# Optimization experiments

Hardware: AMD Instinct MI355X
Metric: run time of the kernel (lower is better)

The kernel has to match this reference:

```python
import jax, jax.numpy as jnp
import numpy as np


def setup_inputs() -> dict:
    key = jax.random.key(0)
    k1, k2 = jax.random.split(key)
    d, T, n = 256, 8192, 64
    # scale down so exp(ht^T D^T D hj) stays in range, as typical trained D would
    H = jax.random.normal(k1, (d, T), dtype=jnp.float32) * 0.1
    D = jax.random.normal(k2, (n, d), dtype=jnp.float32) * 0.1
    l2 = jnp.ones((), dtype=jnp.float32)
    return {"H": H, "D": D, "l2": l2}


def reference(H, D, l2):
    # H: [d, T], D: [n, d]
    DH = D @ H                                   # [n, T] = D @ H_T.T
    # S[t, j] = h_t^T (D^T D) h_j  == (DH)^T (DH)
    S = jnp.einsum('nt,nj->tj', DH, DH)          # [T, T]
    # beta_j = exp(-0.5 * ||D h_j||^2); row t: attn[t,:] = beta * exp(S[t,:]) / sum
    log_beta = -0.5 * jnp.sum(DH * DH, axis=0)   # [T]
    attn_map = jax.nn.softmax(S + log_beta[None, :], axis=1)  # [T, T]
    Z = l2 * (H @ attn_map)                      # [d, T]
    return Z
```

## Files before the change

### kernel.cpp

```cpp
#include <hip/hip_runtime.h>

#define T_DIM 8192
#define D_DIM 256
#define N_DIM 64
#define LOG2E 1.44269504f

typedef __bf16 bf16x8 __attribute__((ext_vector_type(8)));
typedef __bf16 bf16x4 __attribute__((ext_vector_type(4)));
typedef float f32x16 __attribute__((ext_vector_type(16)));

__device__ __forceinline__ f32x16 zero16() {
  f32x16 v;
#pragma unroll
  for (int i = 0; i < 16; ++i) v[i] = 0.f;
  return v;
}


__global__ __launch_bounds__(256) void k_dh(const float* __restrict__ H,
                                            const float* __restrict__ Dm,
                                            __bf16* __restrict__ DHf,
                                            float* __restrict__ lbe,
                                            float* __restrict__ rowsum) {
  __shared__ __bf16 HlThi[64 * 264];
  __shared__ __bf16 HlTlo[64 * 264];
  __shared__ __bf16 DHs[64 * 72];
  const int tid = threadIdx.x;
  const int t0 = blockIdx.x * 64;
  const int lane = tid & 63;
  const int wave = tid >> 6;
  const int h = lane >> 5;
  const int l31 = lane & 31;
  const float4* H4 = (const float4*)H;
#pragma unroll
  for (int r = 0; r < 16; ++r) {
    int idx = r * 256 + tid;
    int d = idx >> 4, tc = idx & 15;
    float4 v = H4[(size_t)d * (T_DIM / 4) + (t0 >> 2) + tc];
    float vv[4] = {v.x, v.y, v.z, v.w};
#pragma unroll
    for (int i = 0; i < 4; ++i) {
      __bf16 hi = (__bf16)vv[i];
      float lo = vv[i] - (float)hi;
      HlThi[(tc * 4 + i) * 264 + d] = hi;
      HlTlo[(tc * 4 + i) * 264 + d] = (__bf16)lo;
    }
  }
  __syncthreads();
  const int tt = wave & 1, nh = wave >> 1;
  const int m = tt * 32 + l31;
  const int n = nh * 32 + l31;
  f32x16 c = zero16();
  for (int kk = 0; kk < 16; ++kk) {
    bf16x8 ahi = *(const bf16x8*)&HlThi[m * 264 + kk * 16 + h * 8];
    bf16x8 alo = *(const bf16x8*)&HlTlo[m * 264 + kk * 16 + h * 8];
    const float4* dp = (const float4*)(Dm + (size_t)n * 256 + kk * 16 + h * 8);
    float4 b0 = dp[0], b1 = dp[1];
    float bv[8] = {b0.x, b0.y, b0.z, b0.w, b1.x, b1.y, b1.z, b1.w};
    bf16x8 bhi, blo;
#pragma unroll
    for (int i = 0; i < 8; ++i) {
      __bf16 hi = (__bf16)bv[i];
      bhi[i] = hi;
      blo[i] = (__bf16)(bv[i] - (float)hi);
    }
    c = __builtin_amdgcn_mfma_f32_32x32x16_bf16(ahi, bhi, c, 0, 0, 0);
    c = __builtin_amdgcn_mfma_f32_32x32x16_bf16(ahi, blo, c, 0, 0, 0);
    c = __builtin_amdgcn_mfma_f32_32x32x16_bf16(alo, bhi, c, 0, 0, 0);
  }
#pragma unroll
  for (int r = 0; r < 16; ++r) {
    int row = tt * 32 + (r & 3) + 8 * (r >> 2) + 4 * h;
    DHs[row * 72 + n] = (__bf16)c[r];
  }
  __syncthreads();
#pragma unroll
  for (int r = 0; r < 2; ++r) {
    int idx = r * 256 + tid;
    int g = idx >> 8, cc = (idx >> 5) & 7, l = idx & 31;
    bf16x8 w = *(const bf16x8*)&DHs[(g * 32 + l) * 72 + cc * 8];
    *(bf16x8*)(DHf + (size_t)(blockIdx.x * 2 + g) * 2048 + cc * 256 + l * 8) = w;
  }
  if (tid < 64) {
    float s = 0.f;
#pragma unroll
    for (int q = 0; q < 8; ++q) {
      bf16x8 w = *(const bf16x8*)&DHs[tid * 72 + q * 8];
#pragma unroll
      for (int i = 0; i < 8; ++i) { float f = (float)w[i]; s += f * f; }
    }
    lbe[t0 + tid] = -0.5f * s * LOG2E;
    rowsum[t0 + tid] = 0.f;
  }
}

__global__ __launch_bounds__(512, 4) void k_rowsum(const __bf16* __restrict__ DHf,
                                                   const float* __restrict__ lbe,
                                                   float* __restrict__ rowsum) {
  __shared__ float red2[256][33];
  const int tid = threadIdx.x;
  const int lane = tid & 63;
  const int wave = tid >> 6;
  const int h = lane >> 5;
  const int l31 = lane & 31;
  const int t0 = (int)(blockIdx.x >> 4) * 256;
  const int jbase = (int)(blockIdx.x & 15) * 512;
  const size_t Gt = (size_t)(t0 >> 5) + wave;
  bf16x8 aR[4];
#pragma unroll
  for (int kk = 0; kk < 4; ++kk)
    aR[kk] = *(const bf16x8*)(DHf + Gt * 2048 + kk * 512 + lane * 8);
  float racc[16];
#pragma unroll
  for (int r = 0; r < 16; ++r) racc[r] = 0.f;
  bf16x8 b[4];
  {
    const size_t Gj = (size_t)(jbase >> 5);
#pragma unroll
    for (int kk = 0; kk < 4; ++kk)
      b[kk] = *(const bf16x8*)(DHf + Gj * 2048 + kk * 512 + lane * 8);
  }
  for (int jit = 0; jit < 16; ++jit) {
    bf16x8 bn[4];
    if (jit < 15) {
      const size_t Gj = (size_t)(jbase >> 5) + jit + 1;
#pragma unroll
      for (int kk = 0; kk < 4; ++kk)
        bn[kk] = *(const bf16x8*)(DHf + Gj * 2048 + kk * 512 + lane * 8);
    }
    const float lbv = lbe[jbase + jit * 32 + l31];
    f32x16 s = zero16();
    s = __builtin_amdgcn_mfma_f32_32x32x16_bf16(aR[0], b[0], s, 0, 0, 0);
    s = __builtin_amdgcn_mfma_f32_32x32x16_bf16(aR[1], b[1], s, 0, 0, 0);
    s = __builtin_amdgcn_mfma_f32_32x32x16_bf16(aR[2], b[2], s, 0, 0, 0);
    s = __builtin_amdgcn_mfma_f32_32x32x16_bf16(aR[3], b[3], s, 0, 0, 0);
#pragma unroll
    for (int r = 0; r < 16; ++r)
      racc[r] += __builtin_amdgcn_exp2f(__builtin_fmaf(s[r], LOG2E, lbv));
    if (jit < 15) {
#pragma unroll
      for (int kk = 0; kk < 4; ++kk) b[kk] = bn[kk];
    }
  }
#pragma unroll
  for (int r = 0; r < 16; ++r) {
    int tl = wave * 32 + (r & 3) + 8 * (r >> 2) + 4 * h;
    red2[tl][l31] = racc[r];
  }
  __syncthreads();
  if (tid < 256) {
    float s = 0.f;
#pragma unroll 8
    for (int c = 0; c < 32; ++c) s += red2[tid][c];
    atomicAdd(&rowsum[t0 + tid], s);
  }
}

__global__ __launch_bounds__(256) void k_scaleH(const float* __restrict__ H,
                                                const float* __restrict__ rowsum,
                                                __bf16* __restrict__ Hbf_sw) {
  __shared__ float rinvL[64];
  const int tid = threadIdx.x;
  const int bx = blockIdx.x;
  const int tblk = bx >> 1, dh = bx & 1;
  const int t0 = tblk * 64;
  if (tid < 64) rinvL[tid] = 1.0f / rowsum[t0 + tid];
  __syncthreads();
#pragma unroll
  for (int itr = 0; itr < 4; ++itr) {
    int idx = itr * 256 + tid;
    int dl = idx >> 3, tbp = idx & 7;
    int d = dh * 128 + dl;
    int swz = (d ^ (d >> 3)) & 7;
    int tloc = (tbp ^ swz) << 3;
    const float4* hp = (const float4*)(H + (size_t)d * T_DIM + t0 + tloc);
    float4 v0 = hp[0], v1 = hp[1];
    float4 r0 = *(const float4*)&rinvL[tloc];
    float4 r1 = *(const float4*)&rinvL[tloc + 4];
    bf16x8 w;
    w[0] = (__bf16)(v0.x * r0.x); w[1] = (__bf16)(v0.y * r0.y);
    w[2] = (__bf16)(v0.z * r0.z); w[3] = (__bf16)(v0.w * r0.w);
    w[4] = (__bf16)(v1.x * r1.x); w[5] = (__bf16)(v1.y * r1.y);
    w[6] = (__bf16)(v1.z * r1.z); w[7] = (__bf16)(v1.w * r1.w);
    *(bf16x8*)(Hbf_sw + (size_t)tblk * 16384 + (size_t)d * 64 + tbp * 8) = w;
  }
}

__global__ __launch_bounds__(256, 2) void k_z(const __bf16* __restrict__ Hbf_sw,
                                              const __bf16* __restrict__ DHf,
                                              const float* __restrict__ lbe,
                                              float* __restrict__ Zp) {
  __shared__ __bf16 Hs[2][128 * 64];
  __shared__ __bf16 Pt[2][128 * 64];
  const int tid = threadIdx.x;
  const int lane = tid & 63;
  const int wave = tid >> 6;
  const int h = lane >> 5;
  const int l31 = lane & 31;
  const int bx = blockIdx.x;
  const int ts = bx & 3;
  const int dh = (bx >> 2) & 1;
  const int j0 = (bx >> 3) * 128;
  const int s_tt = wave & 1, s_jg = wave >> 1;
  bf16x8 bS[2][4];
  float lbv[2];
#pragma unroll
  for (int q = 0; q < 2; ++q) {
    const size_t Gj = (j0 >> 5) + s_jg * 2 + q;
#pragma unroll
    for (int kk = 0; kk < 4; ++kk)
      bS[q][kk] = *(const bf16x8*)(DHf + Gj * 2048 + kk * 512 + lane * 8);
    lbv[q] = lbe[j0 + (s_jg * 2 + q) * 32 + l31];
  }
  f32x16 acc[2][2];
#pragma unroll
  for (int u = 0; u < 2; ++u)
#pragma unroll
    for (int v = 0; v < 2; ++v) acc[u][v] = zero16();

#define DMA_HS(buf_, it_)                                                       \
  {                                                                             \
    const __bf16* gsrc =                                                        \
        Hbf_sw + (size_t)(ts * 32 + (it_)) * 16384 + (size_t)dh * 8192;         \
    _Pragma("unroll") for (int r = 0; r < 4; ++r) {                             \
      int chunk = wave * 4 + r;                                                 \
      __builtin_amdgcn_global_load_lds(                                         \
          (const __attribute__((address_space(1))) unsigned int*)(gsrc +        \
              chunk * 512 + lane * 8),                                          \
          (__attribute__((address_space(3))) unsigned int*)(&Hs[buf_][0] +      \
              chunk * 512),                                                     \
          16, 0, 0);                                                            \
    }                                                                           \
  }

#define LOAD_AR(reg_, n_)                                                       \
  {                                                                             \
    const size_t Gt_ = (size_t)(ts * 64 + (n_)*2 + s_tt);                       \
    _Pragma("unroll") for (int kk = 0; kk < 4; ++kk)                            \
        (reg_)[kk] = *(const bf16x8*)(DHf + Gt_ * 2048 + kk * 512 + lane * 8);  \
  }

#define S_PHASE(p_, reg_)                                                       \
  {                                                                             \
    _Pragma("unroll") for (int q = 0; q < 2; ++q) {                             \
      f32x16 s = zero16();                                                      \
      _Pragma("unroll") for (int kk = 0; kk < 4; ++kk)                          \
          s = __builtin_amdgcn_mfma_f32_32x32x16_bf16((reg_)[kk], bS[q][kk], s, \
                                                      0, 0, 0);                 \
      const int jl = (s_jg * 2 + q) * 32 + l31;                                 \
      const int sj = (jl ^ (jl >> 3)) & 7;                                      \
      _Pragma("unroll") for (int g = 0; g < 4; ++g) {                           \
        const int tl = s_tt * 32 + g * 8 + 4 * h;                               \
        bf16x4 pv;                                                              \
        pv[0] = (__bf16)__builtin_amdgcn_exp2f(                                 \
            __builtin_fmaf(s[g * 4 + 0], LOG2E, lbv[q]));                       \
        pv[1] = (__bf16)__builtin_amdgcn_exp2f(                                 \
            __builtin_fmaf(s[g * 4 + 1], LOG2E, lbv[q]));                       \
        pv[2] = (__bf16)__builtin_amdgcn_exp2f(                                 \
            __builtin_fmaf(s[g * 4 + 2], LOG2E, lbv[q]));                       \
        pv[3] = (__bf16)__builtin_amdgcn_exp2f(                                 \
            __builtin_fmaf(s[g * 4 + 3], LOG2E, lbv[q]));                       \
        const int cchunk = tl >> 3;                                             \
        *(bf16x4*)&Pt[p_][jl * 64 + ((cchunk ^ sj) << 3) + 4 * h] = pv;         \
      }                                                                         \
    }                                                                           \
  }

#define Z_PHASE(p_)                                                             \
  {                                                                             \
    __builtin_amdgcn_s_setprio(1);                                              \
    _Pragma("unroll") for (int kk = 0; kk < 4; ++kk) {                          \
      const int c = kk * 2 + h;                                                 \
      bf16x8 af[2], bw[2];                                                      \
      _Pragma("unroll") for (int u = 0; u < 2; ++u) {                           \
        int dl = (wave & 1) * 64 + u * 32 + l31;                                \
        af[u] =                                                                 \
            *(const bf16x8*)&Hs[p_][dl * 64 + ((c ^ ((dl ^ (dl >> 3)) & 7)) << 3)]; \
      }                                                                         \
      _Pragma("unroll") for (int v = 0; v < 2; ++v) {                           \
        int j = (wave >> 1) * 64 + v * 32 + l31;                                \
        bw[v] =                                                                 \
            *(const bf16x8*)&Pt[p_][j * 64 + ((c ^ ((j ^ (j >> 3)) & 7)) << 3)]; \
      }                                                                         \
      _Pragma("unroll") for (int u = 0; u < 2; ++u)                             \
          _Pragma("unroll") for (int v = 0; v < 2; ++v)                         \
              acc[u][v] = __builtin_amdgcn_mfma_f32_32x32x16_bf16(              \
                  af[u], bw[v], acc[u][v], 0, 0, 0);                            \
    }                                                                           \
    __builtin_amdgcn_s_setprio(0);                                              \
  }

  bf16x8 aR[4], aRn[4];
  LOAD_AR(aR, 0);
  DMA_HS(0, 0);
  S_PHASE(0, aR);
  LOAD_AR(aRn, 1);
  __syncthreads();

  for (int ii = 0; ii < 16; ++ii) {
    const int it0 = ii * 2;
    DMA_HS(1, it0 + 1);
    if (it0 < 30) LOAD_AR(aR, it0 + 2);
    S_PHASE(1, aRn);
    Z_PHASE(0);
    __syncthreads();
    if (it0 + 1 < 31) {
      DMA_HS(0, it0 + 2);
      S_PHASE(0, aR);
    }
    if (it0 + 1 < 30) LOAD_AR(aRn, it0 + 3);
    Z_PHASE(1);
    __syncthreads();
  }
#undef Z_PHASE
#undef S_PHASE
#undef LOAD_AR
#undef DMA_HS
  float* zp = Zp + (size_t)ts * (256 * (size_t)T_DIM);
#pragma unroll
  for (int u = 0; u < 2; ++u)
#pragma unroll
    for (int v = 0; v < 2; ++v)
#pragma unroll
      for (int r = 0; r < 16; ++r) {
        int d = dh * 128 + (wave & 1) * 64 + u * 32 + (r & 3) + 8 * (r >> 2) + 4 * h;
        int j = j0 + (wave >> 1) * 64 + v * 32 + l31;
        zp[(size_t)d * T_DIM + j] = acc[u][v][r];
      }
}

__global__ __launch_bounds__(256) void k_zred(const float* __restrict__ Zp,
                                              const float* __restrict__ l2p,
                                              float* __restrict__ Z) {
  const int i = blockIdx.x * 256 + threadIdx.x;
  const float l2v = l2p[0];
  const float4* zp4 = (const float4*)Zp;
  float4 a = zp4[i];
#pragma unroll
  for (int s = 1; s < 4; ++s) {
    float4 b = zp4[(size_t)s * 524288 + i];
    a.x += b.x; a.y += b.y; a.z += b.z; a.w += b.w;
  }
  float4 o = {a.x * l2v, a.y * l2v, a.z * l2v, a.w * l2v};
  ((float4*)Z)[i] = o;
}

extern "C" void kernel_launch(void* const* d_in, const int* in_sizes, int n_in,
                              void* d_out, int out_size, void* d_ws,
                              size_t ws_size, hipStream_t stream) {
  (void)in_sizes; (void)n_in; (void)out_size; (void)ws_size;
  const float* H = (const float*)d_in[0];
  const float* Dm = (const float*)d_in[1];
  const float* l2 = (const float*)d_in[2];
  float* Z = (float*)d_out;
  char* ws = (char*)d_ws;
  __bf16* DHf = (__bf16*)ws;
  float* lbe = (float*)(ws + 1048576);
  float* rowsum = (float*)(ws + 1048576 + 32768);
  __bf16* Hbf_sw = (__bf16*)(ws + 1114112);
  float* Zp = (float*)(ws + 5308416);

  k_dh<<<128, 256, 0, stream>>>(H, Dm, DHf, lbe, rowsum);
  k_rowsum<<<512, 512, 0, stream>>>(DHf, lbe, rowsum);
  k_scaleH<<<256, 256, 0, stream>>>(H, rowsum, Hbf_sw);
  k_z<<<512, 256, 0, stream>>>(Hbf_sw, DHf, lbe, Zp);
  k_zred<<<2048, 256, 0, stream>>>(Zp, l2, Z);
}
```

Before: 145.7 us.

## Fuse five kernels into one persistent kernel with grid-wide barriers

Merges the DH, rowsum, scale-H, Z and Z-reduction kernels into a single 512-block launch, separating stages with a hierarchical atomic grid barrier. The barrier counters are reset with a memset. The goal is to remove per-kernel launch gaps and tail effects. In exchange, every stage is forced to the same block count and shared-memory union, the DH stage now reads H directly from global memory with strided scalar loads instead of going through LDS, and correctness depends on all 512 blocks being co-resident.

```diff
diff --git a/kernel.cpp b/kernel.cpp
--- a/kernel.cpp
+++ b/kernel.cpp
@@ -16,207 +16,216 @@
   return v;
 }
 
-
-__global__ __launch_bounds__(256) void k_dh(const float* __restrict__ H,
-                                            const float* __restrict__ Dm,
-                                            __bf16* __restrict__ DHf,
-                                            float* __restrict__ lbe,
-                                            float* __restrict__ rowsum) {
-  __shared__ __bf16 HlThi[64 * 264];
-  __shared__ __bf16 HlTlo[64 * 264];
-  __shared__ __bf16 DHs[64 * 72];
+__device__ __forceinline__ void gbar(unsigned int* bar, int slot) {
+  __syncthreads();
+  if (threadIdx.x == 0) {
+    __threadfence();
+    const int bx = (int)blockIdx.x;
+    unsigned int o = __hip_atomic_fetch_add(&bar[16 + slot * 8 + (bx & 7)], 1u,
+                                            __ATOMIC_ACQ_REL,
+                                            __HIP_MEMORY_SCOPE_AGENT);
+    if (o == 63u) {
+      unsigned int r = __hip_atomic_fetch_add(&bar[slot], 1u, __ATOMIC_ACQ_REL,
+                                              __HIP_MEMORY_SCOPE_AGENT);
+      if (r == 7u)
+        __hip_atomic_store(&bar[8 + slot], 1u, __ATOMIC_RELEASE,
+                           __HIP_MEMORY_SCOPE_AGENT);
+    }
+    while (__hip_atomic_load(&bar[8 + slot], __ATOMIC_RELAXED,
+                             __HIP_MEMORY_SCOPE_AGENT) == 0u)
+      __builtin_amdgcn_s_sleep(8);
+    __threadfence();
+  }
+  __syncthreads();
+}
+
+union SMem {
+  struct {
+    __bf16 Hs[2][8192];
+    __bf16 Pt[2][8192];
+  } z;
+  __bf16 DHs[64 * 72];
+  float red2[128][33];
+  float rinvL[64];
+};
+
+__global__ __launch_bounds__(256, 2) void k_fused(
+    const float* __restrict__ H, const float* __restrict__ Dm,
+    const float* __restrict__ l2p, float* __restrict__ Z,
+    __bf16* __restrict__ DHf, float* __restrict__ lbe,
+    float* __restrict__ rowsum, __bf16* __restrict__ Hbf_sw,
+    float* __restrict__ Zp, unsigned int* __restrict__ bar) {
+  __shared__ SMem smem;
   const int tid = threadIdx.x;
-  const int t0 = blockIdx.x * 64;
+  const int bx = (int)blockIdx.x;
   const int lane = tid & 63;
   const int wave = tid >> 6;
   const int h = lane >> 5;
   const int l31 = lane & 31;
-  const float4* H4 = (const float4*)H;
-#pragma unroll
-  for (int r = 0; r < 16; ++r) {
-    int idx = r * 256 + tid;
-    int d = idx >> 4, tc = idx & 15;
-    float4 v = H4[(size_t)d * (T_DIM / 4) + (t0 >> 2) + tc];
-    float vv[4] = {v.x, v.y, v.z, v.w};
-#pragma unroll
-    for (int i = 0; i < 4; ++i) {
-      __bf16 hi = (__bf16)vv[i];
-      float lo = vv[i] - (float)hi;
-      HlThi[(tc * 4 + i) * 264 + d] = hi;
-      HlTlo[(tc * 4 + i) * 264 + d] = (__bf16)lo;
-    }
-  }
-  __syncthreads();
-  const int tt = wave & 1, nh = wave >> 1;
-  const int m = tt * 32 + l31;
-  const int n = nh * 32 + l31;
-  f32x16 c = zero16();
-  for (int kk = 0; kk < 16; ++kk) {
-    bf16x8 ahi = *(const bf16x8*)&HlThi[m * 264 + kk * 16 + h * 8];
-    bf16x8 alo = *(const bf16x8*)&HlTlo[m * 264 + kk * 16 + h * 8];
-    const float4* dp = (const float4*)(Dm + (size_t)n * 256 + kk * 16 + h * 8);
-    float4 b0 = dp[0], b1 = dp[1];
-    float bv[8] = {b0.x, b0.y, b0.z, b0.w, b1.x, b1.y, b1.z, b1.w};
-    bf16x8 bhi, blo;
-#pragma unroll
-    for (int i = 0; i < 8; ++i) {
-      __bf16 hi = (__bf16)bv[i];
-      bhi[i] = hi;
-      blo[i] = (__bf16)(bv[i] - (float)hi);
-    }
-    c = __builtin_amdgcn_mfma_f32_32x32x16_bf16(ahi, bhi, c, 0, 0, 0);
-    c = __builtin_amdgcn_mfma_f32_32x32x16_bf16(ahi, blo, c, 0, 0, 0);
-    c = __builtin_amdgcn_mfma_f32_32x32x16_bf16(alo, bhi, c, 0, 0, 0);
-  }
-#pragma unroll
-  for (int r = 0; r < 16; ++r) {
-    int row = tt * 32 + (r & 3) + 8 * (r >> 2) + 4 * h;
-    DHs[row * 72 + n] = (__bf16)c[r];
-  }
-  __syncthreads();
-#pragma unroll
-  for (int r = 0; r < 2; ++r) {
-    int idx = r * 256 + tid;
-    int g = idx >> 8, cc = (idx >> 5) & 7, l = idx & 31;
-    bf16x8 w = *(const bf16x8*)&DHs[(g * 32 + l) * 72 + cc * 8];
-    *(bf16x8*)(DHf + (size_t)(blockIdx.x * 2 + g) * 2048 + cc * 256 + l * 8) = w;
-  }
-  if (tid < 64) {
-    float s = 0.f;
-#pragma unroll
-    for (int q = 0; q < 8; ++q) {
-      bf16x8 w = *(const bf16x8*)&DHs[tid * 72 + q * 8];
-#pragma unroll
-      for (int i = 0; i < 8; ++i) { float f = (float)w[i]; s += f * f; }
-    }
-    lbe[t0 + tid] = -0.5f * s * LOG2E;
-    rowsum[t0 + tid] = 0.f;
-  }
-}
-
-__global__ __launch_bounds__(512, 4) void k_rowsum(const __bf16* __restrict__ DHf,
-                                                   const float* __restrict__ lbe,
-                                                   float* __restrict__ rowsum) {
-  __shared__ float red2[256][33];
-  const int tid = threadIdx.x;
-  const int lane = tid & 63;
-  const int wave = tid >> 6;
-  const int h = lane >> 5;
-  const int l31 = lane & 31;
-  const int t0 = (int)(blockIdx.x >> 4) * 256;
-  const int jbase = (int)(blockIdx.x & 15) * 512;
-  const size_t Gt = (size_t)(t0 >> 5) + wave;
-  bf16x8 aR[4];
-#pragma unroll
-  for (int kk = 0; kk < 4; ++kk)
-    aR[kk] = *(const bf16x8*)(DHf + Gt * 2048 + kk * 512 + lane * 8);
-  float racc[16];
-#pragma unroll
-  for (int r = 0; r < 16; ++r) racc[r] = 0.f;
-  bf16x8 b[4];
+
+  if (bx < 128) {
+    const int t0 = bx * 64;
+    const int tt = wave & 1, nh = wave >> 1;
+    const int m = tt * 32 + l31;
+    const int n = nh * 32 + l31;
+    f32x16 c = zero16();
+    for (int kk = 0; kk < 16; ++kk) {
+      float av[8];
+#pragma unroll
+      for (int e = 0; e < 8; ++e)
+        av[e] = H[(size_t)(kk * 16 + h * 8 + e) * T_DIM + t0 + m];
+      bf16x8 ahi, alo;
+#pragma unroll
+      for (int e = 0; e < 8; ++e) {
+        __bf16 hi = (__bf16)av[e];
+        ahi[e] = hi;
+        alo[e] = (__bf16)(av[e] - (float)hi);
+      }
+      const float4* dp = (const float4*)(Dm + (size_t)n * 256 + kk * 16 + h * 8);
+      float4 b0 = dp[0], b1 = dp[1];
+      float bv[8] = {b0.x, b0.y, b0.z, b0.w, b1.x, b1.y, b1.z, b1.w};
+      bf16x8 bhi, blo;
+#pragma unroll
+      for (int i = 0; i < 8; ++i) {
+        __bf16 hi = (__bf16)bv[i];
+        bhi[i] = hi;
+        blo[i] = (__bf16)(bv[i] - (float)hi);
+      }
+      c = __builtin_amdgcn_mfma_f32_32x32x16_bf16(ahi, bhi, c, 0, 0, 0);
+      c = __builtin_amdgcn_mfma_f32_32x32x16_bf16(ahi, blo, c, 0, 0, 0);
+      c = __builtin_amdgcn_mfma_f32_32x32x16_bf16(alo, bhi, c, 0, 0, 0);
+    }
+#pragma unroll
+    for (int r = 0; r < 16; ++r) {
+      int row = tt * 32 + (r & 3) + 8 * (r >> 2) + 4 * h;
+      smem.DHs[row * 72 + n] = (__bf16)c[r];
+    }
+    __syncthreads();
+#pragma unroll
+    for (int r = 0; r < 2; ++r) {
+      int idx = r * 256 + tid;
+      int g = idx >> 8, cc = (idx >> 5) & 7, l = idx & 31;
+      bf16x8 w = *(const bf16x8*)&smem.DHs[(g * 32 + l) * 72 + cc * 8];
+      *(bf16x8*)(DHf + (size_t)(bx * 2 + g) * 2048 + cc * 256 + l * 8) = w;
+    }
+    if (tid < 64) {
+      float s = 0.f;
+#pragma unroll
+      for (int q = 0; q < 8; ++q) {
+        bf16x8 w = *(const bf16x8*)&smem.DHs[tid * 72 + q * 8];
+#pragma unroll
+        for (int i = 0; i < 8; ++i) { float f = (float)w[i]; s += f * f; }
+      }
+      lbe[t0 + tid] = -0.5f * s * LOG2E;
+      rowsum[t0 + tid] = 0.f;
+    }
+  }
+  gbar(bar, 0);
+
   {
-    const size_t Gj = (size_t)(jbase >> 5);
+    const int t0 = (bx >> 3) * 128;
+    const int jbase = (bx & 7) * 1024;
+    const size_t Gt = (size_t)(t0 >> 5) + wave;
+    bf16x8 aR[4];
 #pragma unroll
     for (int kk = 0; kk < 4; ++kk)
-      b[kk] = *(const bf16x8*)(DHf + Gj * 2048 + kk * 512 + lane * 8);
-  }
-  for (int jit = 0; jit < 16; ++jit) {
-    bf16x8 bn[4];
-    if (jit < 15) {
-      const size_t Gj = (size_t)(jbase >> 5) + jit + 1;
+      aR[kk] = *(const bf16x8*)(DHf + Gt * 2048 + kk * 512 + lane * 8);
+    float racc[16];
+#pragma unroll
+    for (int r = 0; r < 16; ++r) racc[r] = 0.f;
+    bf16x8 b[4];
+    {
+      const size_t Gj = (size_t)(jbase >> 5);
 #pragma unroll
       for (int kk = 0; kk < 4; ++kk)
-        bn[kk] = *(const bf16x8*)(DHf + Gj * 2048 + kk * 512 + lane * 8);
-    }
-    const float lbv = lbe[jbase + jit * 32 + l31];
-    f32x16 s = zero16();
-    s = __builtin_amdgcn_mfma_f32_32x32x16_bf16(aR[0], b[0], s, 0, 0, 0);
-    s = __builtin_amdgcn_mfma_f32_32x32x16_bf16(aR[1], b[1], s, 0, 0, 0);
-    s = __builtin_amdgcn_mfma_f32_32x32x16_bf16(aR[2], b[2], s, 0, 0, 0);
-    s = __builtin_amdgcn_mfma_f32_32x32x16_bf16(aR[3], b[3], s, 0, 0, 0);
-#pragma unroll
-    for (int r = 0; r < 16; ++r)
-      racc[r] += __builtin_amdgcn_exp2f(__builtin_fmaf(s[r], LOG2E, lbv));
-    if (jit < 15) {
-#pragma unroll
-      for (int kk = 0; kk < 4; ++kk) b[kk] = bn[kk];
-    }
-  }
-#pragma unroll
-  for (int r = 0; r < 16; ++r) {
-    int tl = wave * 32 + (r & 3) + 8 * (r >> 2) + 4 * h;
-    red2[tl][l31] = racc[r];
-  }
-  __syncthreads();
-  if (tid < 256) {
-    float s = 0.f;
+        b[kk] = *(const bf16x8*)(DHf + Gj * 2048 + kk * 512 + lane * 8);
+    }
+    for (int jit = 0; jit < 32; ++jit) {
+      bf16x8 bn[4];
+      if (jit < 31) {
+        const size_t Gj = (size_t)(jbase >> 5) + jit + 1;
+#pragma unroll
+        for (int kk = 0; kk < 4; ++kk)
+          bn[kk] = *(const bf16x8*)(DHf + Gj * 2048 + kk * 512 + lane * 8);
+      }
+      const float lbv = lbe[jbase + jit * 32 + l31];
+      f32x16 s = zero16();
+      s = __builtin_amdgcn_mfma_f32_32x32x16_bf16(aR[0], b[0], s, 0, 0, 0);
+      s = __builtin_amdgcn_mfma_f32_32x32x16_bf16(aR[1], b[1], s, 0, 0, 0);
+      s = __builtin_amdgcn_mfma_f32_32x32x16_bf16(aR[2], b[2], s, 0, 0, 0);
+      s = __builtin_amdgcn_mfma_f32_32x32x16_bf16(aR[3], b[3], s, 0, 0, 0);
+#pragma unroll
+      for (int r = 0; r < 16; ++r)
+        racc[r] += __builtin_amdgcn_exp2f(__builtin_fmaf(s[r], LOG2E, lbv));
+      if (jit < 31) {
+#pragma unroll
+        for (int kk = 0; kk < 4; ++kk) b[kk] = bn[kk];
+      }
+    }
+#pragma unroll
+    for (int r = 0; r < 16; ++r) {
+      int tl = wave * 32 + (r & 3) + 8 * (r >> 2) + 4 * h;
+      smem.red2[tl][l31] = racc[r];
+    }
+    __syncthreads();
+    if (tid < 128) {
+      float s = 0.f;
 #pragma unroll 8
-    for (int c = 0; c < 32; ++c) s += red2[tid][c];
-    atomicAdd(&rowsum[t0 + tid], s);
-  }
-}
-
-__global__ __launch_bounds__(256) void k_scaleH(const float* __restrict__ H,
-                                                const float* __restrict__ rowsum,
-                                                __bf16* __restrict__ Hbf_sw) {
-  __shared__ float rinvL[64];
-  const int tid = threadIdx.x;
-  const int bx = blockIdx.x;
-  const int tblk = bx >> 1, dh = bx & 1;
-  const int t0 = tblk * 64;
-  if (tid < 64) rinvL[tid] = 1.0f / rowsum[t0 + tid];
-  __syncthreads();
-#pragma unroll
-  for (int itr = 0; itr < 4; ++itr) {
-    int idx = itr * 256 + tid;
-    int dl = idx >> 3, tbp = idx & 7;
-    int d = dh * 128 + dl;
-    int swz = (d ^ (d >> 3)) & 7;
-    int tloc = (tbp ^ swz) << 3;
-    const float4* hp = (const float4*)(H + (size_t)d * T_DIM + t0 + tloc);
-    float4 v0 = hp[0], v1 = hp[1];
-    float4 r0 = *(const float4*)&rinvL[tloc];
-    float4 r1 = *(const float4*)&rinvL[tloc + 4];
-    bf16x8 w;
-    w[0] = (__bf16)(v0.x * r0.x); w[1] = (__bf16)(v0.y * r0.y);
-    w[2] = (__bf16)(v0.z * r0.z); w[3] = (__bf16)(v0.w * r0.w);
-    w[4] = (__bf16)(v1.x * r1.x); w[5] = (__bf16)(v1.y * r1.y);
-    w[6] = (__bf16)(v1.z * r1.z); w[7] = (__bf16)(v1.w * r1.w);
-    *(bf16x8*)(Hbf_sw + (size_t)tblk * 16384 + (size_t)d * 64 + tbp * 8) = w;
-  }
-}
-
-__global__ __launch_bounds__(256, 2) void k_z(const __bf16* __restrict__ Hbf_sw,
-                                              const __bf16* __restrict__ DHf,
-                                              const float* __restrict__ lbe,
-                                              float* __restrict__ Zp) {
-  __shared__ __bf16 Hs[2][128 * 64];
-  __shared__ __bf16 Pt[2][128 * 64];
-  const int tid = threadIdx.x;
-  const int lane = tid & 63;
-  const int wave = tid >> 6;
-  const int h = lane >> 5;
-  const int l31 = lane & 31;
-  const int bx = blockIdx.x;
-  const int ts = bx & 3;
-  const int dh = (bx >> 2) & 1;
-  const int j0 = (bx >> 3) * 128;
-  const int s_tt = wave & 1, s_jg = wave >> 1;
-  bf16x8 bS[2][4];
-  float lbv[2];
-#pragma unroll
-  for (int q = 0; q < 2; ++q) {
-    const size_t Gj = (j0 >> 5) + s_jg * 2 + q;
-#pragma unroll
-    for (int kk = 0; kk < 4; ++kk)
-      bS[q][kk] = *(const bf16x8*)(DHf + Gj * 2048 + kk * 512 + lane * 8);
-    lbv[q] = lbe[j0 + (s_jg * 2 + q) * 32 + l31];
-  }
-  f32x16 acc[2][2];
-#pragma unroll
-  for (int u = 0; u < 2; ++u)
-#pragma unroll
-    for (int v = 0; v < 2; ++v) acc[u][v] = zero16();
+      for (int c = 0; c < 32; ++c) s += smem.red2[tid][c];
+      atomicAdd(&rowsum[t0 + tid], s);
+    }
+  }
+  gbar(bar, 1);
+
+  {
+    const int u = bx >> 1;
+    const int tblk = u >> 1, dh = u & 1;
+    const int half = bx & 1;
+    const int t0 = tblk * 64;
+    if (tid < 64) smem.rinvL[tid] = 1.0f / rowsum[t0 + tid];
+    __syncthreads();
+#pragma unroll
+    for (int ii = 0; ii < 2; ++ii) {
+      int itr = half * 2 + ii;
+      int idx = itr * 256 + tid;
+      int dl = idx >> 3, tbp = idx & 7;
+      int d = dh * 128 + dl;
+      int swz = (d ^ (d >> 3)) & 7;
+      int tloc = (tbp ^ swz) << 3;
+      const float4* hp = (const float4*)(H + (size_t)d * T_DIM + t0 + tloc);
+      float4 v0 = hp[0], v1 = hp[1];
+      float4 r0 = *(const float4*)&smem.rinvL[tloc];
+      float4 r1 = *(const float4*)&smem.rinvL[tloc + 4];
+      bf16x8 w;
+      w[0] = (__bf16)(v0.x * r0.x); w[1] = (__bf16)(v0.y * r0.y);
+      w[2] = (__bf16)(v0.z * r0.z); w[3] = (__bf16)(v0.w * r0.w);
+      w[4] = (__bf16)(v1.x * r1.x); w[5] = (__bf16)(v1.y * r1.y);
+      w[6] = (__bf16)(v1.z * r1.z); w[7] = (__bf16)(v1.w * r1.w);
+      *(bf16x8*)(Hbf_sw + (size_t)tblk * 16384 + (size_t)d * 64 + tbp * 8) = w;
+    }
+  }
+  gbar(bar, 2);
+
+  {
+    const int ts = bx & 3;
+    const int dh = (bx >> 2) & 1;
+    const int j0 = (bx >> 3) * 128;
+    const int s_tt = wave & 1, s_jg = wave >> 1;
+    bf16x8 bS[2][4];
+    float lbv[2];
+#pragma unroll
+    for (int q = 0; q < 2; ++q) {
+      const size_t Gj = (j0 >> 5) + s_jg * 2 + q;
+#pragma unroll
+      for (int kk = 0; kk < 4; ++kk)
+        bS[q][kk] = *(const bf16x8*)(DHf + Gj * 2048 + kk * 512 + lane * 8);
+      lbv[q] = lbe[j0 + (s_jg * 2 + q) * 32 + l31];
+    }
+    f32x16 acc[2][2];
+#pragma unroll
+    for (int u = 0; u < 2; ++u)
+#pragma unroll
+      for (int v = 0; v < 2; ++v) acc[u][v] = zero16();
 
 #define DMA_HS(buf_, it_)                                                       \
   {                                                                             \
@@ -227,7 +236,7 @@
       __builtin_amdgcn_global_load_lds(                                         \
           (const __attribute__((address_space(1))) unsigned int*)(gsrc +        \
               chunk * 512 + lane * 8),                                          \
-          (__attribute__((address_space(3))) unsigned int*)(&Hs[buf_][0] +      \
+          (__attribute__((address_space(3))) unsigned int*)(&smem.z.Hs[buf_][0] + \
               chunk * 512),                                                     \
           16, 0, 0);                                                            \
     }                                                                           \
@@ -261,7 +270,7 @@
         pv[3] = (__bf16)__builtin_amdgcn_exp2f(                                 \
             __builtin_fmaf(s[g * 4 + 3], LOG2E, lbv[q]));                       \
         const int cchunk = tl >> 3;                                             \
-        *(bf16x4*)&Pt[p_][jl * 64 + ((cchunk ^ sj) << 3) + 4 * h] = pv;         \
+        *(bf16x4*)&smem.z.Pt[p_][jl * 64 + ((cchunk ^ sj) << 3) + 4 * h] = pv;  \
       }                                                                         \
     }                                                                           \
   }
@@ -274,13 +283,13 @@
       bf16x8 af[2], bw[2];                                                      \
       _Pragma("unroll") for (int u = 0; u < 2; ++u) {                           \
         int dl = (wave & 1) * 64 + u * 32 + l31;                                \
-        af[u] =                                                                 \
-            *(const bf16x8*)&Hs[p_][dl * 64 + ((c ^ ((dl ^ (dl >> 3)) & 7)) << 3)]; \
+        af[u] = *(const bf16x8*)&smem.z                                         \
+                     .Hs[p_][dl * 64 + ((c ^ ((dl ^ (dl >> 3)) & 7)) << 3)];    \
       }                                                                         \
       _Pragma("unroll") for (int v = 0; v < 2; ++v) {                           \
         int j = (wave >> 1) * 64 + v * 32 + l31;                                \
-        bw[v] =                                                                 \
-            *(const bf16x8*)&Pt[p_][j * 64 + ((c ^ ((j ^ (j >> 3)) & 7)) << 3)]; \
+        bw[v] = *(const bf16x8*)&smem.z                                         \
+                     .Pt[p_][j * 64 + ((c ^ ((j ^ (j >> 3)) & 7)) << 3)];       \
       }                                                                         \
       _Pragma("unroll") for (int u = 0; u < 2; ++u)                             \
           _Pragma("unroll") for (int v = 0; v < 2; ++v)                         \
@@ -290,59 +299,63 @@
     __builtin_amdgcn_s_setprio(0);                                              \
   }
 
-  bf16x8 aR[4], aRn[4];
-  LOAD_AR(aR, 0);
-  DMA_HS(0, 0);
-  S_PHASE(0, aR);
-  LOAD_AR(aRn, 1);
-  __syncthreads();
-
-  for (int ii = 0; ii < 16; ++ii) {
-    const int it0 = ii * 2;
-    DMA_HS(1, it0 + 1);
-    if (it0 < 30) LOAD_AR(aR, it0 + 2);
-    S_PHASE(1, aRn);
-    Z_PHASE(0);
+    bf16x8 aR[4], aRn[4];
+    LOAD_AR(aR, 0);
+    DMA_HS(0, 0);
+    S_PHASE(0, aR);
+    LOAD_AR(aRn, 1);
     __syncthreads();
-    if (it0 + 1 < 31) {
-      DMA_HS(0, it0 + 2);
-      S_PHASE(0, aR);
-    }
-    if (it0 + 1 < 30) LOAD_AR(aRn, it0 + 3);
-    Z_PHASE(1);
-    __syncthreads();
-  }
+
+    for (int ii = 0; ii < 16; ++ii) {
+      const int it0 = ii * 2;
+      DMA_HS(1, it0 + 1);
+      if (it0 < 30) LOAD_AR(aR, it0 + 2);
+      S_PHASE(1, aRn);
+      Z_PHASE(0);
+      __syncthreads();
+      if (it0 + 1 < 31) {
+        DMA_HS(0, it0 + 2);
+        S_PHASE(0, aR);
+      }
+      if (it0 + 1 < 30) LOAD_AR(aRn, it0 + 3);
+      Z_PHASE(1);
+      __syncthreads();
+    }
 #undef Z_PHASE
 #undef S_PHASE
 #undef LOAD_AR
 #undef DMA_HS
-  float* zp = Zp + (size_t)ts * (256 * (size_t)T_DIM);
-#pragma unroll
-  for (int u = 0; u < 2; ++u)
-#pragma unroll
-    for (int v = 0; v < 2; ++v)
-#pragma unroll
-      for (int r = 0; r < 16; ++r) {
-        int d = dh * 128 + (wave & 1) * 64 + u * 32 + (r & 3) + 8 * (r >> 2) + 4 * h;
-        int j = j0 + (wave >> 1) * 64 + v * 32 + l31;
-        zp[(size_t)d * T_DIM + j] = acc[u][v][r];
-      }
-}
-
-__global__ __launch_bounds__(256) void k_zred(const float* __restrict__ Zp,
-                                              const float* __restrict__ l2p,
-                                              float* __restrict__ Z) {
-  const int i = blockIdx.x * 256 + threadIdx.x;
-  const float l2v = l2p[0];
-  const float4* zp4 = (const float4*)Zp;
-  float4 a = zp4[i];
-#pragma unroll
-  for (int s = 1; s < 4; ++s) {
-    float4 b = zp4[(size_t)s * 524288 + i];
-    a.x += b.x; a.y += b.y; a.z += b.z; a.w += b.w;
-  }
-  float4 o = {a.x * l2v, a.y * l2v, a.z * l2v, a.w * l2v};
-  ((float4*)Z)[i] = o;
+    float* zp = Zp + (size_t)ts * (256 * (size_t)T_DIM);
+#pragma unroll
+    for (int u = 0; u < 2; ++u)
+#pragma unroll
+      for (int v = 0; v < 2; ++v)
+#pragma unroll
+        for (int r = 0; r < 16; ++r) {
+          int d = dh * 128 + (wave & 1) * 64 + u * 32 + (r & 3) + 8 * (r >> 2) + 4 * h;
+          int j = j0 + (wave >> 1) * 64 + v * 32 + l31;
+          zp[(size_t)d * T_DIM + j] = acc[u][v][r];
+        }
+  }
+  gbar(bar, 3);
+
+  {
+    const float l2v = l2p[0];
+    const float4* zp4 = (const float4*)Zp;
+    float4* Z4 = (float4*)Z;
+#pragma unroll
+    for (int k = 0; k < 4; ++k) {
+      int i = k * 131072 + bx * 256 + tid;
+      float4 a = zp4[i];
+#pragma unroll
+      for (int s = 1; s < 4; ++s) {
+        float4 b = zp4[(size_t)s * 524288 + i];
+        a.x += b.x; a.y += b.y; a.z += b.z; a.w += b.w;
+      }
+      float4 o = {a.x * l2v, a.y * l2v, a.z * l2v, a.w * l2v};
+      Z4[i] = o;
+    }
+  }
 }
 
 extern "C" void kernel_launch(void* const* d_in, const int* in_sizes, int n_in,
@@ -356,13 +369,12 @@
   char* ws = (char*)d_ws;
   __bf16* DHf = (__bf16*)ws;
   float* lbe = (float*)(ws + 1048576);
-  float* rowsum = (float*)(ws + 1048576 + 32768);
-  __bf16* Hbf_sw = (__bf16*)(ws + 1114112);
-  float* Zp = (float*)(ws + 5308416);
-
-  k_dh<<<128, 256, 0, stream>>>(H, Dm, DHf, lbe, rowsum);
-  k_rowsum<<<512, 512, 0, stream>>>(DHf, lbe, rowsum);
-  k_scaleH<<<256, 256, 0, stream>>>(H, rowsum, Hbf_sw);
-  k_z<<<512, 256, 0, stream>>>(Hbf_sw, DHf, lbe, Zp);
-  k_zred<<<2048, 256, 0, stream>>>(Zp, l2, Z);
+  float* rowsum = (float*)(ws + 1081344);
+  unsigned int* bar = (unsigned int*)(ws + 1114112);
+  __bf16* Hbf_sw = (__bf16*)(ws + 1114624);
+  float* Zp = (float*)(ws + 5308928);
+
+  hipMemsetAsync(bar, 0, 512, stream);
+  k_fused<<<512, 256, 0, stream>>>(H, Dm, l2, Z, DHf, lbe, rowsum, Hbf_sw, Zp,
+                                   bar);
 }
```

Result: slower. 339.1 us (+132.7%).

## Fold H bf16 conversion into k_dh and apply row normalisation inside k_z

Applied to the files above, without the earlier changes.

Removes the separate k_scaleH launch. The plain bf16 conversion of H now runs as extra blocks of k_dh, since it no longer depends on rowsum. The 1/rowsum scaling moves into k_z's S phase, where each probability is multiplied by a reciprocal loaded from rowsum before it is stored to LDS. This saves one kernel launch and one pass over H, at the cost of extra rowsum loads, rcp and multiplies per tile inside the main kernel.

```diff
diff --git a/kernel.cpp b/kernel.cpp
--- a/kernel.cpp
+++ b/kernel.cpp
@@ -21,16 +21,42 @@
                                             const float* __restrict__ Dm,
                                             __bf16* __restrict__ DHf,
                                             float* __restrict__ lbe,
-                                            float* __restrict__ rowsum) {
+                                            float* __restrict__ rowsum,
+                                            __bf16* __restrict__ Hbf) {
   __shared__ __bf16 HlThi[64 * 264];
   __shared__ __bf16 HlTlo[64 * 264];
   __shared__ __bf16 DHs[64 * 72];
   const int tid = threadIdx.x;
-  const int t0 = blockIdx.x * 64;
+  const int bx = (int)blockIdx.x;
   const int lane = tid & 63;
   const int wave = tid >> 6;
   const int h = lane >> 5;
   const int l31 = lane & 31;
+
+  if (bx >= 128) {
+    const int cbx = bx - 128;
+    const int tblk = cbx >> 1, dh2 = cbx & 1;
+    const int t0c = tblk * 64;
+#pragma unroll
+    for (int itr = 0; itr < 4; ++itr) {
+      int idx = itr * 256 + tid;
+      int dl = idx >> 3, tbp = idx & 7;
+      int d = dh2 * 128 + dl;
+      int swz = (d ^ (d >> 3)) & 7;
+      int tloc = (tbp ^ swz) << 3;
+      const float4* hp = (const float4*)(H + (size_t)d * T_DIM + t0c + tloc);
+      float4 v0 = hp[0], v1 = hp[1];
+      bf16x8 w;
+      w[0] = (__bf16)v0.x; w[1] = (__bf16)v0.y;
+      w[2] = (__bf16)v0.z; w[3] = (__bf16)v0.w;
+      w[4] = (__bf16)v1.x; w[5] = (__bf16)v1.y;
+      w[6] = (__bf16)v1.z; w[7] = (__bf16)v1.w;
+      *(bf16x8*)(Hbf + (size_t)tblk * 16384 + (size_t)d * 64 + tbp * 8) = w;
+    }
+    return;
+  }
+
+  const int t0 = bx * 64;
   const float4* H4 = (const float4*)H;
 #pragma unroll
   for (int r = 0; r < 16; ++r) {
@@ -79,7 +105,7 @@
     int idx = r * 256 + tid;
     int g = idx >> 8, cc = (idx >> 5) & 7, l = idx & 31;
     bf16x8 w = *(const bf16x8*)&DHs[(g * 32 + l) * 72 + cc * 8];
-    *(bf16x8*)(DHf + (size_t)(blockIdx.x * 2 + g) * 2048 + cc * 256 + l * 8) = w;
+    *(bf16x8*)(DHf + (size_t)(bx * 2 + g) * 2048 + cc * 256 + l * 8) = w;
   }
   if (tid < 64) {
     float s = 0.f;
@@ -156,39 +182,10 @@
   }
 }
 
-__global__ __launch_bounds__(256) void k_scaleH(const float* __restrict__ H,
-                                                const float* __restrict__ rowsum,
-                                                __bf16* __restrict__ Hbf_sw) {
-  __shared__ float rinvL[64];
-  const int tid = threadIdx.x;
-  const int bx = blockIdx.x;
-  const int tblk = bx >> 1, dh = bx & 1;
-  const int t0 = tblk * 64;
-  if (tid < 64) rinvL[tid] = 1.0f / rowsum[t0 + tid];
-  __syncthreads();
-#pragma unroll
-  for (int itr = 0; itr < 4; ++itr) {
-    int idx = itr * 256 + tid;
-    int dl = idx >> 3, tbp = idx & 7;
-    int d = dh * 128 + dl;
-    int swz = (d ^ (d >> 3)) & 7;
-    int tloc = (tbp ^ swz) << 3;
-    const float4* hp = (const float4*)(H + (size_t)d * T_DIM + t0 + tloc);
-    float4 v0 = hp[0], v1 = hp[1];
-    float4 r0 = *(const float4*)&rinvL[tloc];
-    float4 r1 = *(const float4*)&rinvL[tloc + 4];
-    bf16x8 w;
-    w[0] = (__bf16)(v0.x * r0.x); w[1] = (__bf16)(v0.y * r0.y);
-    w[2] = (__bf16)(v0.z * r0.z); w[3] = (__bf16)(v0.w * r0.w);
-    w[4] = (__bf16)(v1.x * r1.x); w[5] = (__bf16)(v1.y * r1.y);
-    w[6] = (__bf16)(v1.z * r1.z); w[7] = (__bf16)(v1.w * r1.w);
-    *(bf16x8*)(Hbf_sw + (size_t)tblk * 16384 + (size_t)d * 64 + tbp * 8) = w;
-  }
-}
-
-__global__ __launch_bounds__(256, 2) void k_z(const __bf16* __restrict__ Hbf_sw,
+__global__ __launch_bounds__(256, 2) void k_z(const __bf16* __restrict__ Hbf,
                                               const __bf16* __restrict__ DHf,
                                               const float* __restrict__ lbe,
+                                              const float* __restrict__ rowsum,
                                               float* __restrict__ Zp) {
   __shared__ __bf16 Hs[2][128 * 64];
   __shared__ __bf16 Pt[2][128 * 64];
@@ -221,7 +218,7 @@
 #define DMA_HS(buf_, it_)                                                       \
   {                                                                             \
     const __bf16* gsrc =                                                        \
-        Hbf_sw + (size_t)(ts * 32 + (it_)) * 16384 + (size_t)dh * 8192;         \
+        Hbf + (size_t)(ts * 32 + (it_)) * 16384 + (size_t)dh * 8192;            \
     _Pragma("unroll") for (int r = 0; r < 4; ++r) {                             \
       int chunk = wave * 4 + r;                                                 \
       __builtin_amdgcn_global_load_lds(                                         \
@@ -240,8 +237,17 @@
         (reg_)[kk] = *(const bf16x8*)(DHf + Gt_ * 2048 + kk * 512 + lane * 8);  \
   }
 
-#define S_PHASE(p_, reg_)                                                       \
+#define S_PHASE(p_, reg_, n_)                                                   \
   {                                                                             \
+    const int rsb_ = ((ts * 32 + (n_)) << 6) + s_tt * 32 + 4 * h;               \
+    float rv_[16];                                                              \
+    _Pragma("unroll") for (int g = 0; g < 4; ++g) {                             \
+      float4 rr = *(const float4*)&rowsum[rsb_ + g * 8];                        \
+      rv_[g * 4 + 0] = __builtin_amdgcn_rcpf(rr.x);                             \
+      rv_[g * 4 + 1] = __builtin_amdgcn_rcpf(rr.y);                             \
+      rv_[g * 4 + 2] = __builtin_amdgcn_rcpf(rr.z);                             \
+      rv_[g * 4 + 3] = __builtin_amdgcn_rcpf(rr.w);                             \
+    }                                                                           \
     _Pragma("unroll") for (int q = 0; q < 2; ++q) {                             \
       f32x16 s = zero16();                                                      \
       _Pragma("unroll") for (int kk = 0; kk < 4; ++kk)                          \
@@ -252,14 +258,14 @@
       _Pragma("unroll") for (int g = 0; g < 4; ++g) {                           \
         const int tl = s_tt * 32 + g * 8 + 4 * h;                               \
         bf16x4 pv;                                                              \
-        pv[0] = (__bf16)__builtin_amdgcn_exp2f(                                 \
-            __builtin_fmaf(s[g * 4 + 0], LOG2E, lbv[q]));                       \
-        pv[1] = (__bf16)__builtin_amdgcn_exp2f(                                 \
-            __builtin_fmaf(s[g * 4 + 1], LOG2E, lbv[q]));                       \
-        pv[2] = (__bf16)__builtin_amdgcn_exp2f(                                 \
-            __builtin_fmaf(s[g * 4 + 2], LOG2E, lbv[q]));                       \
-        pv[3] = (__bf16)__builtin_amdgcn_exp2f(                                 \
-            __builtin_fmaf(s[g * 4 + 3], LOG2E, lbv[q]));                       \
+        pv[0] = (__bf16)(__builtin_amdgcn_exp2f(                                \
+            __builtin_fmaf(s[g * 4 + 0], LOG2E, lbv[q])) * rv_[g * 4 + 0]);     \
+        pv[1] = (__bf16)(__builtin_amdgcn_exp2f(                                \
+            __builtin_fmaf(s[g * 4 + 1], LOG2E, lbv[q])) * rv_[g * 4 + 1]);     \
+        pv[2] = (__bf16)(__builtin_amdgcn_exp2f(                                \
+            __builtin_fmaf(s[g * 4 + 2], LOG2E, lbv[q])) * rv_[g * 4 + 2]);     \
+        pv[3] = (__bf16)(__builtin_amdgcn_exp2f(                                \
+            __builtin_fmaf(s[g * 4 + 3], LOG2E, lbv[q])) * rv_[g * 4 + 3]);     \
         const int cchunk = tl >> 3;                                             \
         *(bf16x4*)&Pt[p_][jl * 64 + ((cchunk ^ sj) << 3) + 4 * h] = pv;         \
       }                                                                         \
@@ -293,7 +299,7 @@
   bf16x8 aR[4], aRn[4];
   LOAD_AR(aR, 0);
   DMA_HS(0, 0);
-  S_PHASE(0, aR);
+  S_PHASE(0, aR, 0);
   LOAD_AR(aRn, 1);
   __syncthreads();
 
@@ -301,12 +307,12 @@
     const int it0 = ii * 2;
     DMA_HS(1, it0 + 1);
     if (it0 < 30) LOAD_AR(aR, it0 + 2);
-    S_PHASE(1, aRn);
+    S_PHASE(1, aRn, it0 + 1);
     Z_PHASE(0);
     __syncthreads();
     if (it0 + 1 < 31) {
       DMA_HS(0, it0 + 2);
-      S_PHASE(0, aR);
+      S_PHASE(0, aR, it0 + 2);
     }
     if (it0 + 1 < 30) LOAD_AR(aRn, it0 + 3);
     Z_PHASE(1);
@@ -357,12 +363,11 @@
   __bf16* DHf = (__bf16*)ws;
   float* lbe = (float*)(ws + 1048576);
   float* rowsum = (float*)(ws + 1048576 + 32768);
-  __bf16* Hbf_sw = (__bf16*)(ws + 1114112);
+  __bf16* Hbf = (__bf16*)(ws + 1114112);
   float* Zp = (float*)(ws + 5308416);
 
-  k_dh<<<128, 256, 0, stream>>>(H, Dm, DHf, lbe, rowsum);
+  k_dh<<<384, 256, 0, stream>>>(H, Dm, DHf, lbe, rowsum, Hbf);
   k_rowsum<<<512, 512, 0, stream>>>(DHf, lbe, rowsum);
-  k_scaleH<<<256, 256, 0, stream>>>(H, rowsum, Hbf_sw);
-  k_z<<<512, 256, 0, stream>>>(Hbf_sw, DHf, lbe, Zp);
+  k_z<<<512, 256, 0, stream>>>(Hbf, DHf, lbe, rowsum, Zp);
   k_zred<<<2048, 256, 0, stream>>>(Zp, l2, Z);
 }
```

Result: slower. 151.1 us (+3.7%).

## Fuse scaleH and Z reduction into preceding kernels via last-block counters

Applied to the files above, without the earlier changes.

Removes the separate k_scaleH and k_zred launches. The last block to finish a 256-row tile of k_rowsum, detected with an atomic counter, now does the H scaling and bf16 conversion for that tile. The last of the four t-split blocks in k_z sums the partial Z tiles and applies l2. This saves two launches and the gaps between them, at the cost of a memset for the counters, tail work done by a few blocks with less parallelism, and extra fences.

```diff
diff --git a/kernel.cpp b/kernel.cpp
--- a/kernel.cpp
+++ b/kernel.cpp
@@ -96,8 +96,13 @@
 
 __global__ __launch_bounds__(512, 4) void k_rowsum(const __bf16* __restrict__ DHf,
                                                    const float* __restrict__ lbe,
-                                                   float* __restrict__ rowsum) {
+                                                   float* __restrict__ rowsum,
+                                                   const float* __restrict__ H,
+                                                   __bf16* __restrict__ Hbf_sw,
+                                                   unsigned int* __restrict__ cnt) {
   __shared__ float red2[256][33];
+  __shared__ float rinvL[256];
+  __shared__ int isLast;
   const int tid = threadIdx.x;
   const int lane = tid & 63;
   const int wave = tid >> 6;
@@ -154,42 +159,53 @@
     for (int c = 0; c < 32; ++c) s += red2[tid][c];
     atomicAdd(&rowsum[t0 + tid], s);
   }
-}
-
-__global__ __launch_bounds__(256) void k_scaleH(const float* __restrict__ H,
-                                                const float* __restrict__ rowsum,
-                                                __bf16* __restrict__ Hbf_sw) {
-  __shared__ float rinvL[64];
-  const int tid = threadIdx.x;
-  const int bx = blockIdx.x;
-  const int tblk = bx >> 1, dh = bx & 1;
-  const int t0 = tblk * 64;
-  if (tid < 64) rinvL[tid] = 1.0f / rowsum[t0 + tid];
-  __syncthreads();
-#pragma unroll
-  for (int itr = 0; itr < 4; ++itr) {
-    int idx = itr * 256 + tid;
-    int dl = idx >> 3, tbp = idx & 7;
-    int d = dh * 128 + dl;
-    int swz = (d ^ (d >> 3)) & 7;
-    int tloc = (tbp ^ swz) << 3;
-    const float4* hp = (const float4*)(H + (size_t)d * T_DIM + t0 + tloc);
-    float4 v0 = hp[0], v1 = hp[1];
-    float4 r0 = *(const float4*)&rinvL[tloc];
-    float4 r1 = *(const float4*)&rinvL[tloc + 4];
-    bf16x8 w;
-    w[0] = (__bf16)(v0.x * r0.x); w[1] = (__bf16)(v0.y * r0.y);
-    w[2] = (__bf16)(v0.z * r0.z); w[3] = (__bf16)(v0.w * r0.w);
-    w[4] = (__bf16)(v1.x * r1.x); w[5] = (__bf16)(v1.y * r1.y);
-    w[6] = (__bf16)(v1.z * r1.z); w[7] = (__bf16)(v1.w * r1.w);
-    *(bf16x8*)(Hbf_sw + (size_t)tblk * 16384 + (size_t)d * 64 + tbp * 8) = w;
+  __syncthreads();
+  if (tid == 0) {
+    __threadfence();
+    unsigned int old = atomicAdd(&cnt[blockIdx.x >> 4], 1u);
+    isLast = (old == 15u) ? 1 : 0;
+  }
+  __syncthreads();
+  if (isLast) {
+    if (tid == 0) __threadfence();
+    __syncthreads();
+    if (tid < 256)
+      rinvL[tid] = 1.0f / __hip_atomic_load(&rowsum[t0 + tid], __ATOMIC_RELAXED,
+                                            __HIP_MEMORY_SCOPE_AGENT);
+    __syncthreads();
+    const int tb0 = t0 >> 6;
+#pragma unroll
+    for (int pass = 0; pass < 16; ++pass) {
+      int gidx = pass * 512 + tid;
+      int tbl = gidx >> 11;
+      int rem = gidx & 2047;
+      int d = rem >> 3, tbp = rem & 7;
+      int swz = (d ^ (d >> 3)) & 7;
+      int tloc = (tbp ^ swz) << 3;
+      const float4* hp =
+          (const float4*)(H + (size_t)d * T_DIM + (tb0 + tbl) * 64 + tloc);
+      float4 v0 = hp[0], v1 = hp[1];
+      const float* rl = &rinvL[tbl * 64 + tloc];
+      float4 r0 = *(const float4*)rl;
+      float4 r1 = *(const float4*)(rl + 4);
+      bf16x8 w;
+      w[0] = (__bf16)(v0.x * r0.x); w[1] = (__bf16)(v0.y * r0.y);
+      w[2] = (__bf16)(v0.z * r0.z); w[3] = (__bf16)(v0.w * r0.w);
+      w[4] = (__bf16)(v1.x * r1.x); w[5] = (__bf16)(v1.y * r1.y);
+      w[6] = (__bf16)(v1.z * r1.z); w[7] = (__bf16)(v1.w * r1.w);
+      *(bf16x8*)(Hbf_sw + (size_t)(tb0 + tbl) * 16384 + (size_t)d * 64 +
+                 tbp * 8) = w;
+    }
   }
 }
 
 __global__ __launch_bounds__(256, 2) void k_z(const __bf16* __restrict__ Hbf_sw,
                                               const __bf16* __restrict__ DHf,
                                               const float* __restrict__ lbe,
-                                              float* __restrict__ Zp) {
+                                              const float* __restrict__ l2p,
+                                              float* __restrict__ Zp,
+                                              float* __restrict__ Z,
+                                              unsigned int* __restrict__ cnt2) {
   __shared__ __bf16 Hs[2][128 * 64];
   __shared__ __bf16 Pt[2][128 * 64];
   const int tid = threadIdx.x;
@@ -327,22 +343,35 @@
         int j = j0 + (wave >> 1) * 64 + v * 32 + l31;
         zp[(size_t)d * T_DIM + j] = acc[u][v][r];
       }
-}
-
-__global__ __launch_bounds__(256) void k_zred(const float* __restrict__ Zp,
-                                              const float* __restrict__ l2p,
-                                              float* __restrict__ Z) {
-  const int i = blockIdx.x * 256 + threadIdx.x;
-  const float l2v = l2p[0];
-  const float4* zp4 = (const float4*)Zp;
-  float4 a = zp4[i];
-#pragma unroll
-  for (int s = 1; s < 4; ++s) {
-    float4 b = zp4[(size_t)s * 524288 + i];
-    a.x += b.x; a.y += b.y; a.z += b.z; a.w += b.w;
-  }
-  float4 o = {a.x * l2v, a.y * l2v, a.z * l2v, a.w * l2v};
-  ((float4*)Z)[i] = o;
+  __syncthreads();
+  int* flagp = (int*)&Hs[0][0];
+  if (tid == 0) {
+    __threadfence();
+    unsigned int old = atomicAdd(&cnt2[bx >> 2], 1u);
+    *flagp = (old == 3u) ? 1 : 0;
+  }
+  __syncthreads();
+  if (*flagp) {
+    if (tid == 0) __threadfence();
+    __syncthreads();
+    const float l2v = l2p[0];
+    const float4* zp4 = (const float4*)Zp;
+    float4* Z4 = (float4*)Z;
+    const int jq = (j0 >> 2) + (tid & 31);
+#pragma unroll
+    for (int pass = 0; pass < 16; ++pass) {
+      int d = dh * 128 + pass * 8 + (tid >> 5);
+      size_t rowq = (size_t)d * (T_DIM / 4) + jq;
+      float4 a = zp4[rowq];
+#pragma unroll
+      for (int s = 1; s < 4; ++s) {
+        float4 b = zp4[(size_t)s * 524288 + rowq];
+        a.x += b.x; a.y += b.y; a.z += b.z; a.w += b.w;
+      }
+      float4 o = {a.x * l2v, a.y * l2v, a.z * l2v, a.w * l2v};
+      Z4[rowq] = o;
+    }
+  }
 }
 
 extern "C" void kernel_launch(void* const* d_in, const int* in_sizes, int n_in,
@@ -356,13 +385,14 @@
   char* ws = (char*)d_ws;
   __bf16* DHf = (__bf16*)ws;
   float* lbe = (float*)(ws + 1048576);
-  float* rowsum = (float*)(ws + 1048576 + 32768);
-  __bf16* Hbf_sw = (__bf16*)(ws + 1114112);
-  float* Zp = (float*)(ws + 5308416);
-
+  float* rowsum = (float*)(ws + 1081344);
+  unsigned int* cnt = (unsigned int*)(ws + 1114112);
+  unsigned int* cnt2 = (unsigned int*)(ws + 1114240);
+  __bf16* Hbf_sw = (__bf16*)(ws + 1118208);
+  float* Zp = (float*)(ws + 5312512);
+
+  hipMemsetAsync(ws + 1114112, 0, 1024, stream);
   k_dh<<<128, 256, 0, stream>>>(H, Dm, DHf, lbe, rowsum);
-  k_rowsum<<<512, 512, 0, stream>>>(DHf, lbe, rowsum);
-  k_scaleH<<<256, 256, 0, stream>>>(H, rowsum, Hbf_sw);
-  k_z<<<512, 256, 0, stream>>>(Hbf_sw, DHf, lbe, Zp);
-  k_zred<<<2048, 256, 0, stream>>>(Zp, l2, Z);
-}
+  k_rowsum<<<512, 512, 0, stream>>>(DHf, lbe, rowsum, H, Hbf_sw, cnt);
+  k_z<<<512, 256, 0, stream>>>(Hbf_sw, DHf, lbe, l2, Zp, Z, cnt2);
+}
```

Measured after the change: 197.1 us. 35.3% more time.
